# Kernel tuning notes

Hardware: AMD Instinct MI355X
Metric: run time of the kernel (lower is better)

The kernel has to match this reference:

```python
import jax, jax.numpy as jnp
import numpy as np

HEADS = 16
SCALE = 8.0
EPS = 1e-12  # F.normalize eps for fp32


def _l2norm(t):
    # F.normalize(t, dim=-1): t / max(||t||, eps)
    n = jnp.sqrt(jnp.sum(t * t, axis=-1, keepdims=True))
    return t / jnp.maximum(n, EPS)


def setup_inputs() -> dict:
    key = jax.random.key(0)
    k0, k1, k2, k3, k4 = jax.random.split(key, 5)
    b, n, d = 1, 4096, 1024
    w_scale = 1.0 / np.sqrt(d)
    return {
        "x": jax.random.normal(k0, (b, n, d), dtype=jnp.float32),
        "Wq": jax.random.normal(k1, (d, d), dtype=jnp.float32) * w_scale,
        "Wk": jax.random.normal(k2, (d, d), dtype=jnp.float32) * w_scale,
        "Wv": jax.random.normal(k3, (d, d), dtype=jnp.float32) * w_scale,
        "Wo": jax.random.normal(k4, (d, d), dtype=jnp.float32) * w_scale,
    }


def reference(x, Wq, Wk, Wv, Wo):
    b, n, d = x.shape
    h = HEADS
    dh = d // h
    # projections (nn.Linear without bias): y = x @ W  (W stored as [in, out])
    def proj(W):
        y = jnp.einsum('bnd,df->bnf', x, W)
        return y.reshape(b, n, h, dh).transpose(0, 2, 1, 3)  # b h n dh
    q, k, v = proj(Wq), proj(Wk), proj(Wv)
    # cosine-sim attention: L2-normalize q, k along head dim
    q = _l2norm(q)
    k = _l2norm(k)
    sim = jnp.einsum('bhid,bhjd->bhij', q, k) * SCALE
    mask_value = -jnp.finfo(sim.dtype).max
    causal = jnp.triu(jnp.ones((n, n), dtype=bool), 1)
    sim = jnp.where(causal, mask_value, sim)
    attn = jax.nn.softmax(sim, axis=-1)
    o = jnp.einsum('bhij,bhjd->bhid', attn, v)
    o = o.transpose(0, 2, 1, 3).reshape(b, n, d)  # b n (h dh)
    return jnp.einsum('bnf,fd->bnd', o, Wo)
```

## Files before the change

kernel.cpp:

```cpp
#include <hip/hip_runtime.h>
#include <stdint.h>
#include <math.h>

typedef __bf16 bf16_t;
typedef __attribute__((ext_vector_type(8))) __bf16 bf16x8;
typedef __attribute__((ext_vector_type(4))) __bf16 bf16x4;
typedef __attribute__((ext_vector_type(4))) float f32x4;

#define N_TOK 4096
#define D_MODEL 1024
#define HEADS 16
#define DH 64
#define C1 11.541560327111707f
#define C2 11.721897207207671f

__device__ __forceinline__ void async_copy16(const void* g, void* l) {
    __builtin_amdgcn_global_load_lds(
        (const __attribute__((address_space(1))) unsigned int*)g,
        (__attribute__((address_space(3))) unsigned int*)l, 16, 0, 0);
}

__global__ __launch_bounds__(256) void cast_x_kernel(const float* __restrict__ x,
                                                     bf16_t* __restrict__ xb) {
    int i = (blockIdx.x * 256 + threadIdx.x) * 4;
    float4 v = *(const float4*)(x + i);
    bf16x4 o;
    o[0] = (bf16_t)v.x; o[1] = (bf16_t)v.y; o[2] = (bf16_t)v.z; o[3] = (bf16_t)v.w;
    *(bf16x4*)(xb + i) = o;
}

__global__ __launch_bounds__(256) void transpose_w_kernel(
    const float* __restrict__ W0, const float* __restrict__ W1,
    const float* __restrict__ W2, const float* __restrict__ W3,
    bf16_t* __restrict__ T0, bf16_t* __restrict__ T1,
    bf16_t* __restrict__ T2, bf16_t* __restrict__ T3) {
    __shared__ bf16_t t[64][72];
    const float* W; bf16_t* T;
    switch (blockIdx.z) {
        case 0: W = W0; T = T0; break;
        case 1: W = W1; T = T1; break;
        case 2: W = W2; T = T2; break;
        default: W = W3; T = T3; break;
    }
    int k0 = blockIdx.x * 64, n0 = blockIdx.y * 64;
    int tx = threadIdx.x & 63, ty = threadIdx.x >> 6;
#pragma unroll
    for (int i = 0; i < 16; i++) {
        int kl = ty * 16 + i;
        t[kl][tx] = (bf16_t)W[(size_t)(k0 + kl) * D_MODEL + n0 + tx];
    }
    __syncthreads();
#pragma unroll
    for (int i = 0; i < 16; i++) {
        int nl = ty * 16 + i;
        T[(size_t)(n0 + nl) * D_MODEL + k0 + tx] = t[tx][nl];
    }
}

template <int WRITE_F32, int NORM>
__global__ __launch_bounds__(256) void gemm_tile(const bf16_t* __restrict__ A,
                                                 const bf16_t* __restrict__ Bt,
                                                 void* __restrict__ Cout, int ldc) {
    constexpr int K = D_MODEL;
    __shared__ __align__(16) bf16_t As[128 * 32];
    __shared__ __align__(16) bf16_t Bs[128 * 32];
    const int tid = threadIdx.x;
    const int m0 = blockIdx.y * 128;
    const int n0 = blockIdx.x * 128;
    const int wave = tid >> 6;
    const int lane = tid & 63;
    const int l15 = lane & 15;
    const int quad = lane >> 4;
    const int wm = (wave >> 1) * 64;
    const int wn = (wave & 1) * 64;
    f32x4 acc[4][4] = {};

    const int srow = tid >> 2;
    const int soff = (tid & 3) * 8;
    const bf16_t* gA = A + (size_t)(m0 + srow) * K + soff;
    const bf16_t* gB = Bt + (size_t)(n0 + srow) * K + soff;
    bf16_t* lA = &As[tid * 8];
    bf16_t* lB = &Bs[tid * 8];
    constexpr int HGAP = 64 * K;

    for (int kt = 0; kt < K; kt += 32) {
        __syncthreads();
        async_copy16(gA + kt, lA);
        async_copy16(gA + HGAP + kt, lA + 2048);
        async_copy16(gB + kt, lB);
        async_copy16(gB + HGAP + kt, lB + 2048);
        __syncthreads();
        bf16x8 af[4], bfr[4];
#pragma unroll
        for (int mi = 0; mi < 4; mi++)
            af[mi] = *(const bf16x8*)(&As[(wm + mi * 16 + l15) * 32 + quad * 8]);
#pragma unroll
        for (int ni = 0; ni < 4; ni++)
            bfr[ni] = *(const bf16x8*)(&Bs[(wn + ni * 16 + l15) * 32 + quad * 8]);
#pragma unroll
        for (int mi = 0; mi < 4; mi++)
#pragma unroll
            for (int ni = 0; ni < 4; ni++)
                acc[mi][ni] = __builtin_amdgcn_mfma_f32_16x16x32_bf16(
                    af[mi], bfr[ni], acc[mi][ni], 0, 0, 0);
    }

    if (NORM && n0 < 2048) {
#pragma unroll
        for (int mi = 0; mi < 4; mi++)
#pragma unroll
            for (int r = 0; r < 4; r++) {
                float s = 0.f;
#pragma unroll
                for (int ni = 0; ni < 4; ni++) {
                    float v = acc[mi][ni][r];
                    s += v * v;
                }
                s += __shfl_xor(s, 1);
                s += __shfl_xor(s, 2);
                s += __shfl_xor(s, 4);
                s += __shfl_xor(s, 8);
                float sc = 1.0f / fmaxf(sqrtf(s), 1e-12f);
#pragma unroll
                for (int ni = 0; ni < 4; ni++) acc[mi][ni][r] *= sc;
            }
    }
#pragma unroll
    for (int mi = 0; mi < 4; mi++)
#pragma unroll
        for (int ni = 0; ni < 4; ni++)
#pragma unroll
            for (int r = 0; r < 4; r++) {
                int row = m0 + wm + mi * 16 + quad * 4 + r;
                int col = n0 + wn + ni * 16 + l15;
                float v = acc[mi][ni][r];
                if (WRITE_F32)
                    ((float*)Cout)[(size_t)row * ldc + col] = v;
                else
                    ((bf16_t*)Cout)[(size_t)row * ldc + col] = (bf16_t)v;
            }
}

__global__ __launch_bounds__(256) void transpose_v_kernel(const bf16_t* __restrict__ QKV,
                                                          bf16_t* __restrict__ Vt) {
    __shared__ bf16_t t[64][72];
    int n0 = blockIdx.x * 64;
    int h = blockIdx.y;
    int tx = threadIdx.x & 63, ty = threadIdx.x >> 6;
#pragma unroll
    for (int i = 0; i < 16; i++) {
        int nl = ty * 16 + i;
        t[nl][tx] = QKV[(size_t)(n0 + nl) * 3072 + 2048 + h * DH + tx];
    }
    __syncthreads();
    const int e = tx & 7, q = (tx >> 3) & 3;
    const int J = (tx & 32) + 16 * (e >> 2) + 4 * q + (e & 3);
#pragma unroll
    for (int i = 0; i < 16; i++) {
        int dl = ty * 16 + i;
        Vt[(size_t)(h * DH + dl) * N_TOK + n0 + tx] = t[J][dl];
    }
}

__global__ __launch_bounds__(256) void attn_kernel(const bf16_t* __restrict__ QKV,
                                                   const bf16_t* __restrict__ Vt,
                                                   bf16_t* __restrict__ O) {
    __shared__ __align__(16) bf16_t Ks[2][4096];
    __shared__ __align__(16) bf16_t Vs[2][2][2048];
    const int tid = threadIdx.x;
    const int wave = tid >> 6;
    const int lane = tid & 63;
    const int l15 = lane & 15;
    const int quad = lane >> 4;

    const int xcd = blockIdx.x & 7;
    const int t = blockIdx.x >> 3;
    const int h = xcd * 2 + (t & 1);
    const int u = t >> 1;

    const bf16_t* Qb = QKV + h * DH;
    const bf16_t* Kb = QKV + 1024 + h * DH;
    const bf16_t* Vb = Vt + (size_t)h * DH * N_TOK;

    const int krow = tid >> 3;
    const int kc = (tid & 7) ^ (krow & 7);
    const bf16_t* gK = Kb + (size_t)krow * 3072 + kc * 8;
    const int vd = tid >> 2;
    const int vc = (tid & 3) ^ ((vd >> 1) & 3);
    const bf16_t* gV = Vb + (size_t)vd * N_TOK + vc * 8;

    const int ksw = l15 & 7;
    const int vsw = (l15 >> 1) & 3;

    for (int ph = 0; ph < 2; ph++) {
        const int g = ph ? u : 63 - u;
        const int i0 = g * 64 + wave * 16;

        bf16x8 aq[2];
#pragma unroll
        for (int kd = 0; kd < 2; kd++)
            aq[kd] = *(const bf16x8*)(Qb + (size_t)(i0 + l15) * 3072 + kd * 32 + quad * 8);

        f32x4 od[4] = {};
        float l_acc = 0.f;

        if (ph) __syncthreads();
        async_copy16(gK, &Ks[0][tid * 8]);
        async_copy16(gK + (size_t)32 * 3072, &Ks[0][tid * 8 + 2048]);
        async_copy16(gV, &Vs[0][0][tid * 8]);
        async_copy16(gV + 32, &Vs[0][1][tid * 8]);

        for (int jt = 0; jt <= g; jt++) {
            __syncthreads();
            if (jt < g) {
                const int b = (jt + 1) & 1;
                const bf16_t* kn = gK + (size_t)(jt + 1) * 64 * 3072;
                async_copy16(kn, &Ks[b][tid * 8]);
                async_copy16(kn + (size_t)32 * 3072, &Ks[b][tid * 8 + 2048]);
                async_copy16(gV + (jt + 1) * 64, &Vs[b][0][tid * 8]);
                async_copy16(gV + (jt + 1) * 64 + 32, &Vs[b][1][tid * 8]);
            }
            const bf16_t* KS = Ks[jt & 1];
            const bool diag = (jt == g);
            const int jh_max = diag ? wave : 3;

            bf16x8 ak[4][2];
#pragma unroll
            for (int jh = 0; jh < 4; jh++) {
                if (jh > jh_max) continue;
#pragma unroll
                for (int kd = 0; kd < 2; kd++)
                    ak[jh][kd] = *(const bf16x8*)(&KS[(jh * 16 + l15) * 64 +
                                                      (((kd * 4 + quad) ^ ksw) * 8)]);
            }
            f32x4 sj[4] = {};
#pragma unroll
            for (int kd = 0; kd < 2; kd++)
#pragma unroll
                for (int jh = 0; jh < 4; jh++) {
                    if (jh > jh_max) continue;
                    sj[jh] = __builtin_amdgcn_mfma_f32_16x16x32_bf16(ak[jh][kd], aq[kd], sj[jh], 0, 0, 0);
                }

            float p[4][4] = {};
#pragma unroll
            for (int jh = 0; jh < 4; jh++) {
                if (jh > jh_max) continue;
                if (diag && jh == wave) {
#pragma unroll
                    for (int r = 0; r < 4; r++) {
                        float v = (quad * 4 + r > l15) ? 0.f
                                  : __builtin_amdgcn_exp2f(sj[jh][r] * C1 - C2);
                        p[jh][r] = v;
                        l_acc += v;
                    }
                } else {
#pragma unroll
                    for (int r = 0; r < 4; r++) {
                        float v = __builtin_amdgcn_exp2f(sj[jh][r] * C1 - C2);
                        p[jh][r] = v;
                        l_acc += v;
                    }
                }
            }
            bf16x8 pk8[2];
#pragma unroll
            for (int H = 0; H < 2; H++)
#pragma unroll
                for (int r = 0; r < 4; r++) {
                    pk8[H][r] = (bf16_t)p[2 * H][r];
                    pk8[H][4 + r] = (bf16_t)p[2 * H + 1][r];
                }

            const bf16_t* VS0 = Vs[jt & 1][0];
#pragma unroll
            for (int mt = 0; mt < 4; mt++) {
                bf16x8 vf = *(const bf16x8*)(&VS0[(mt * 16 + l15) * 32 + ((quad ^ vsw) * 8)]);
                od[mt] = __builtin_amdgcn_mfma_f32_16x16x32_bf16(vf, pk8[0], od[mt], 0, 0, 0);
            }
            if (jh_max >= 2) {
                const bf16_t* VS1 = Vs[jt & 1][1];
#pragma unroll
                for (int mt = 0; mt < 4; mt++) {
                    bf16x8 vf = *(const bf16x8*)(&VS1[(mt * 16 + l15) * 32 + ((quad ^ vsw) * 8)]);
                    od[mt] = __builtin_amdgcn_mfma_f32_16x16x32_bf16(vf, pk8[1], od[mt], 0, 0, 0);
                }
            }
        }

        float l = l_acc;
        l += __shfl_xor(l, 16);
        l += __shfl_xor(l, 32);
        float inv = 1.0f / l;

#pragma unroll
        for (int mt = 0; mt < 4; mt++) {
            bf16x4 o;
#pragma unroll
            for (int r = 0; r < 4; r++) o[r] = (bf16_t)(od[mt][r] * inv);
            *(bf16x4*)(&O[(size_t)(i0 + l15) * D_MODEL + h * DH + mt * 16 + quad * 4]) = o;
        }
    }
}

extern "C" void kernel_launch(void* const* d_in, const int* in_sizes, int n_in,
                              void* d_out, int out_size, void* d_ws, size_t ws_size,
                              hipStream_t stream) {
    const float* x  = (const float*)d_in[0];
    const float* Wq = (const float*)d_in[1];
    const float* Wk = (const float*)d_in[2];
    const float* Wv = (const float*)d_in[3];
    const float* Wo = (const float*)d_in[4];
    float* out = (float*)d_out;
    char* ws = (char*)d_ws;
    const size_t MB = 1024 * 1024;
    bf16_t* xb   = (bf16_t*)(ws);
    bf16_t* Wt3  = (bf16_t*)(ws + 8 * MB);
    bf16_t* Wot  = (bf16_t*)(ws + 14 * MB);
    bf16_t* QKV  = (bf16_t*)(ws + 16 * MB);
    bf16_t* Vt   = (bf16_t*)(ws + 40 * MB);
    bf16_t* Ob   = (bf16_t*)(ws + 48 * MB);

    cast_x_kernel<<<4096, 256, 0, stream>>>(x, xb);
    dim3 gw(16, 16, 4);
    transpose_w_kernel<<<gw, 256, 0, stream>>>(Wq, Wk, Wv, Wo,
                                               Wt3, Wt3 + 1024 * 1024, Wt3 + 2 * 1024 * 1024, Wot);
    dim3 gqkv(3072 / 128, N_TOK / 128);
    gemm_tile<0, 1><<<gqkv, 256, 0, stream>>>(xb, Wt3, QKV, 3072);
    dim3 gv(N_TOK / 64, HEADS);
    transpose_v_kernel<<<gv, 256, 0, stream>>>(QKV, Vt);
    attn_kernel<<<512, 256, 0, stream>>>(QKV, Vt, Ob);
    dim3 go(D_MODEL / 128, N_TOK / 128);
    gemm_tile<1, 0><<<go, 256, 0, stream>>>(Ob, Wot, out, D_MODEL);
}
```

Baseline: 208.2 us.

## Process heavy and light causal query tiles concurrently with shared K/V stream

```diff
diff --git a/kernel.cpp b/kernel.cpp
--- a/kernel.cpp
+++ b/kernel.cpp
@@ -174,13 +174,34 @@
     const int quad = lane >> 4;
 
     const int xcd = blockIdx.x & 7;
-    const int t = blockIdx.x >> 3;
-    const int h = xcd * 2 + (t & 1);
-    const int u = t >> 1;
+    const int hb = (blockIdx.x >> 3) & 1;
+    const int jj = (blockIdx.x >> 4) & 15;
+    const int ph2 = blockIdx.x >> 8;
+    const int h = xcd * 2 + hb;
+    const int u = ph2 ? 31 - jj : jj;
+    const int g1 = 63 - u;
+    const int g0 = u;
+
+    const bool heavy = wave < 2;
+    const int wg = wave & 1;
+    const int g_my = heavy ? g1 : g0;
+    const int ib0 = wg * 2;
+    const int i_base = g_my * 64 + wg * 32;
 
     const bf16_t* Qb = QKV + h * DH;
     const bf16_t* Kb = QKV + 1024 + h * DH;
     const bf16_t* Vb = Vt + (size_t)h * DH * N_TOK;
+
+    bf16x8 aq[2][2];
+#pragma unroll
+    for (int s = 0; s < 2; s++)
+#pragma unroll
+        for (int kd = 0; kd < 2; kd++)
+            aq[s][kd] = *(const bf16x8*)(Qb + (size_t)(i_base + s * 16 + l15) * 3072 +
+                                         kd * 32 + quad * 8);
+
+    f32x4 od[2][4] = {};
+    float l_acc[2] = {0.f, 0.f};
 
     const int krow = tid >> 3;
     const int kc = (tid & 7) ^ (krow & 7);
@@ -189,116 +210,118 @@
     const int vc = (tid & 3) ^ ((vd >> 1) & 3);
     const bf16_t* gV = Vb + (size_t)vd * N_TOK + vc * 8;
 
+    async_copy16(gK, &Ks[0][tid * 8]);
+    async_copy16(gK + (size_t)32 * 3072, &Ks[0][tid * 8 + 2048]);
+    async_copy16(gV, &Vs[0][0][tid * 8]);
+    async_copy16(gV + 32, &Vs[0][1][tid * 8]);
+
     const int ksw = l15 & 7;
     const int vsw = (l15 >> 1) & 3;
 
-    for (int ph = 0; ph < 2; ph++) {
-        const int g = ph ? u : 63 - u;
-        const int i0 = g * 64 + wave * 16;
-
-        bf16x8 aq[2];
+    for (int jt = 0; jt <= g1; jt++) {
+        __syncthreads();
+        if (jt < g1) {
+            const int b = (jt + 1) & 1;
+            const bf16_t* kn = gK + (size_t)(jt + 1) * 64 * 3072;
+            async_copy16(kn, &Ks[b][tid * 8]);
+            async_copy16(kn + (size_t)32 * 3072, &Ks[b][tid * 8 + 2048]);
+            async_copy16(gV + (jt + 1) * 64, &Vs[b][0][tid * 8]);
+            async_copy16(gV + (jt + 1) * 64 + 32, &Vs[b][1][tid * 8]);
+        }
+        if (!heavy && jt > g0) continue;
+        const bf16_t* KS = Ks[jt & 1];
+        const bool diag = (jt == g_my);
+        const int jm0 = diag ? ib0 : 3;
+        const int jm1 = diag ? ib0 + 1 : 3;
+
+        bf16x8 ak[4][2];
+#pragma unroll
+        for (int jh = 0; jh < 4; jh++) {
+            if (jh > jm1) continue;
+#pragma unroll
+            for (int kd = 0; kd < 2; kd++)
+                ak[jh][kd] = *(const bf16x8*)(&KS[(jh * 16 + l15) * 64 +
+                                                  (((kd * 4 + quad) ^ ksw) * 8)]);
+        }
+        f32x4 sj[2][4] = {};
 #pragma unroll
         for (int kd = 0; kd < 2; kd++)
-            aq[kd] = *(const bf16x8*)(Qb + (size_t)(i0 + l15) * 3072 + kd * 32 + quad * 8);
-
-        f32x4 od[4] = {};
-        float l_acc = 0.f;
-
-        if (ph) __syncthreads();
-        async_copy16(gK, &Ks[0][tid * 8]);
-        async_copy16(gK + (size_t)32 * 3072, &Ks[0][tid * 8 + 2048]);
-        async_copy16(gV, &Vs[0][0][tid * 8]);
-        async_copy16(gV + 32, &Vs[0][1][tid * 8]);
-
-        for (int jt = 0; jt <= g; jt++) {
-            __syncthreads();
-            if (jt < g) {
-                const int b = (jt + 1) & 1;
-                const bf16_t* kn = gK + (size_t)(jt + 1) * 64 * 3072;
-                async_copy16(kn, &Ks[b][tid * 8]);
-                async_copy16(kn + (size_t)32 * 3072, &Ks[b][tid * 8 + 2048]);
-                async_copy16(gV + (jt + 1) * 64, &Vs[b][0][tid * 8]);
-                async_copy16(gV + (jt + 1) * 64 + 32, &Vs[b][1][tid * 8]);
-            }
-            const bf16_t* KS = Ks[jt & 1];
-            const bool diag = (jt == g);
-            const int jh_max = diag ? wave : 3;
-
-            bf16x8 ak[4][2];
+#pragma unroll
+            for (int jh = 0; jh < 4; jh++)
+#pragma unroll
+                for (int s = 0; s < 2; s++) {
+                    if (jh > (diag ? ib0 + s : 3)) continue;
+                    sj[s][jh] = __builtin_amdgcn_mfma_f32_16x16x32_bf16(
+                        ak[jh][kd], aq[s][kd], sj[s][jh], 0, 0, 0);
+                }
+
+        float p[2][4][4] = {};
+#pragma unroll
+        for (int s = 0; s < 2; s++) {
 #pragma unroll
             for (int jh = 0; jh < 4; jh++) {
-                if (jh > jh_max) continue;
-#pragma unroll
-                for (int kd = 0; kd < 2; kd++)
-                    ak[jh][kd] = *(const bf16x8*)(&KS[(jh * 16 + l15) * 64 +
-                                                      (((kd * 4 + quad) ^ ksw) * 8)]);
-            }
-            f32x4 sj[4] = {};
-#pragma unroll
-            for (int kd = 0; kd < 2; kd++)
-#pragma unroll
-                for (int jh = 0; jh < 4; jh++) {
-                    if (jh > jh_max) continue;
-                    sj[jh] = __builtin_amdgcn_mfma_f32_16x16x32_bf16(ak[jh][kd], aq[kd], sj[jh], 0, 0, 0);
-                }
-
-            float p[4][4] = {};
-#pragma unroll
-            for (int jh = 0; jh < 4; jh++) {
-                if (jh > jh_max) continue;
-                if (diag && jh == wave) {
+                if (jh > (diag ? ib0 + s : 3)) continue;
+                if (diag && jh == ib0 + s) {
 #pragma unroll
                     for (int r = 0; r < 4; r++) {
                         float v = (quad * 4 + r > l15) ? 0.f
-                                  : __builtin_amdgcn_exp2f(sj[jh][r] * C1 - C2);
-                        p[jh][r] = v;
-                        l_acc += v;
+                                  : __builtin_amdgcn_exp2f(sj[s][jh][r] * C1 - C2);
+                        p[s][jh][r] = v;
+                        l_acc[s] += v;
                     }
                 } else {
 #pragma unroll
                     for (int r = 0; r < 4; r++) {
-                        float v = __builtin_amdgcn_exp2f(sj[jh][r] * C1 - C2);
-                        p[jh][r] = v;
-                        l_acc += v;
+                        float v = __builtin_amdgcn_exp2f(sj[s][jh][r] * C1 - C2);
+                        p[s][jh][r] = v;
+                        l_acc[s] += v;
                     }
                 }
             }
-            bf16x8 pk8[2];
+        }
+        bf16x8 pk8[2][2];
+#pragma unroll
+        for (int s = 0; s < 2; s++)
 #pragma unroll
             for (int H = 0; H < 2; H++)
 #pragma unroll
                 for (int r = 0; r < 4; r++) {
-                    pk8[H][r] = (bf16_t)p[2 * H][r];
-                    pk8[H][4 + r] = (bf16_t)p[2 * H + 1][r];
+                    pk8[s][H][r] = (bf16_t)p[s][2 * H][r];
+                    pk8[s][H][4 + r] = (bf16_t)p[s][2 * H + 1][r];
                 }
 
-            const bf16_t* VS0 = Vs[jt & 1][0];
+        const bf16_t* VS0 = Vs[jt & 1][0];
+#pragma unroll
+        for (int mt = 0; mt < 4; mt++) {
+            bf16x8 vf = *(const bf16x8*)(&VS0[(mt * 16 + l15) * 32 + ((quad ^ vsw) * 8)]);
+            od[0][mt] = __builtin_amdgcn_mfma_f32_16x16x32_bf16(vf, pk8[0][0], od[0][mt], 0, 0, 0);
+            od[1][mt] = __builtin_amdgcn_mfma_f32_16x16x32_bf16(vf, pk8[1][0], od[1][mt], 0, 0, 0);
+        }
+        if (jm1 >= 2) {
+            const bf16_t* VS1 = Vs[jt & 1][1];
 #pragma unroll
             for (int mt = 0; mt < 4; mt++) {
-                bf16x8 vf = *(const bf16x8*)(&VS0[(mt * 16 + l15) * 32 + ((quad ^ vsw) * 8)]);
-                od[mt] = __builtin_amdgcn_mfma_f32_16x16x32_bf16(vf, pk8[0], od[mt], 0, 0, 0);
+                bf16x8 vf = *(const bf16x8*)(&VS1[(mt * 16 + l15) * 32 + ((quad ^ vsw) * 8)]);
+                if (jm0 >= 2)
+                    od[0][mt] = __builtin_amdgcn_mfma_f32_16x16x32_bf16(vf, pk8[0][1], od[0][mt], 0, 0, 0);
+                od[1][mt] = __builtin_amdgcn_mfma_f32_16x16x32_bf16(vf, pk8[1][1], od[1][mt], 0, 0, 0);
             }
-            if (jh_max >= 2) {
-                const bf16_t* VS1 = Vs[jt & 1][1];
-#pragma unroll
-                for (int mt = 0; mt < 4; mt++) {
-                    bf16x8 vf = *(const bf16x8*)(&VS1[(mt * 16 + l15) * 32 + ((quad ^ vsw) * 8)]);
-                    od[mt] = __builtin_amdgcn_mfma_f32_16x16x32_bf16(vf, pk8[1], od[mt], 0, 0, 0);
-                }
-            }
-        }
-
-        float l = l_acc;
+        }
+    }
+
+#pragma unroll
+    for (int s = 0; s < 2; s++) {
+        float l = l_acc[s];
         l += __shfl_xor(l, 16);
         l += __shfl_xor(l, 32);
         float inv = 1.0f / l;
-
 #pragma unroll
         for (int mt = 0; mt < 4; mt++) {
             bf16x4 o;
 #pragma unroll
-            for (int r = 0; r < 4; r++) o[r] = (bf16_t)(od[mt][r] * inv);
-            *(bf16x4*)(&O[(size_t)(i0 + l15) * D_MODEL + h * DH + mt * 16 + quad * 4]) = o;
+            for (int r = 0; r < 4; r++) o[r] = (bf16_t)(od[s][mt][r] * inv);
+            *(bf16x4*)(&O[(size_t)(i_base + s * 16 + l15) * D_MODEL + h * DH +
+                          mt * 16 + quad * 4]) = o;
         }
     }
 }
```

Result: slower. 246.5 us (+18.4%).

## Fold softmax scale into Q normalization and compute row sums via MFMA

Applied to the files above, without the earlier changes.

```diff
diff --git a/kernel.cpp b/kernel.cpp
--- a/kernel.cpp
+++ b/kernel.cpp
@@ -12,7 +12,6 @@
 #define HEADS 16
 #define DH 64
 #define C1 11.541560327111707f
-#define C2 11.721897207207671f
 
 __device__ __forceinline__ void async_copy16(const void* g, void* l) {
     __builtin_amdgcn_global_load_lds(
@@ -106,6 +105,7 @@
     }
 
     if (NORM && n0 < 2048) {
+        const float post = (n0 < 1024) ? C1 : 1.0f;
 #pragma unroll
         for (int mi = 0; mi < 4; mi++)
 #pragma unroll
@@ -120,7 +120,7 @@
                 s += __shfl_xor(s, 2);
                 s += __shfl_xor(s, 4);
                 s += __shfl_xor(s, 8);
-                float sc = 1.0f / fmaxf(sqrtf(s), 1e-12f);
+                float sc = post / fmaxf(sqrtf(s), 1e-12f);
 #pragma unroll
                 for (int ni = 0; ni < 4; ni++) acc[mi][ni][r] *= sc;
             }
@@ -192,6 +192,10 @@
     const int ksw = l15 & 7;
     const int vsw = (l15 >> 1) & 3;
 
+    bf16x8 vone;
+#pragma unroll
+    for (int i = 0; i < 8; i++) vone[i] = (bf16_t)1.0f;
+
     for (int ph = 0; ph < 2; ph++) {
         const int g = ph ? u : 63 - u;
         const int i0 = g * 64 + wave * 16;
@@ -202,7 +206,7 @@
             aq[kd] = *(const bf16x8*)(Qb + (size_t)(i0 + l15) * 3072 + kd * 32 + quad * 8);
 
         f32x4 od[4] = {};
-        float l_acc = 0.f;
+        f32x4 lv = {};
 
         if (ph) __syncthreads();
         async_copy16(gK, &Ks[0][tid * 8]);
@@ -248,19 +252,13 @@
                 if (jh > jh_max) continue;
                 if (diag && jh == wave) {
 #pragma unroll
-                    for (int r = 0; r < 4; r++) {
-                        float v = (quad * 4 + r > l15) ? 0.f
-                                  : __builtin_amdgcn_exp2f(sj[jh][r] * C1 - C2);
-                        p[jh][r] = v;
-                        l_acc += v;
-                    }
+                    for (int r = 0; r < 4; r++)
+                        p[jh][r] = (quad * 4 + r > l15) ? 0.f
+                                   : __builtin_amdgcn_exp2f(sj[jh][r]);
                 } else {
 #pragma unroll
-                    for (int r = 0; r < 4; r++) {
-                        float v = __builtin_amdgcn_exp2f(sj[jh][r] * C1 - C2);
-                        p[jh][r] = v;
-                        l_acc += v;
-                    }
+                    for (int r = 0; r < 4; r++)
+                        p[jh][r] = __builtin_amdgcn_exp2f(sj[jh][r]);
                 }
             }
             bf16x8 pk8[2];
@@ -272,6 +270,10 @@
                     pk8[H][4 + r] = (bf16_t)p[2 * H + 1][r];
                 }
 
+            lv = __builtin_amdgcn_mfma_f32_16x16x32_bf16(vone, pk8[0], lv, 0, 0, 0);
+            if (jh_max >= 2)
+                lv = __builtin_amdgcn_mfma_f32_16x16x32_bf16(vone, pk8[1], lv, 0, 0, 0);
+
             const bf16_t* VS0 = Vs[jt & 1][0];
 #pragma unroll
             for (int mt = 0; mt < 4; mt++) {
@@ -288,10 +290,7 @@
             }
         }
 
-        float l = l_acc;
-        l += __shfl_xor(l, 16);
-        l += __shfl_xor(l, 32);
-        float inv = 1.0f / l;
+        float inv = 1.0f / lv[0];
 
 #pragma unroll
         for (int mt = 0; mt < 4; mt++) {
```

After: 209.9 us. Within noise of the previous version (+0.8%).
